# Optimization experiments

Hardware: AMD Instinct MI355X
Metric: run time of the kernel (lower is better)

## Reference

```python
import jax, jax.numpy as jnp
import numpy as np

H = 2048       # hidden_size
NH = 16        # num_attention_heads
HN = H // NH   # per-head dim = 128
B = 2
S = 2048
ALPHA = 32.0   # cogview pb-relax alpha


def setup_inputs() -> dict:
    key = jax.random.key(0)
    k1, k2, k3 = jax.random.split(key, 3)
    hidden_states = jax.random.normal(k1, (B, S, H), dtype=jnp.float32)
    # causal lower-triangular float mask [1,1,s,s]
    ltor_mask = jnp.tril(jnp.ones((S, S), dtype=jnp.float32))[None, None]
    # fused QKV projection params (torch Linear: y = x @ W.T + b)
    lim_qkv = 1.0 / np.sqrt(H)
    W_qkv = jax.random.uniform(k2, (3 * H, H), jnp.float32, -lim_qkv, lim_qkv)
    b_qkv = jnp.zeros((3 * H,), jnp.float32)
    W_out = jax.random.uniform(k3, (H, H), jnp.float32, -lim_qkv, lim_qkv)
    b_out = jnp.zeros((H,), jnp.float32)
    return {"hidden_states": hidden_states, "ltor_mask": ltor_mask,
            "W_qkv": W_qkv, "b_qkv": b_qkv, "W_out": W_out, "b_out": b_out}


def reference(hidden_states, ltor_mask, W_qkv, b_qkv, W_out, b_out):
    b, s, h = hidden_states.shape
    # fused QKV projection: [b,s,3h]
    qkv = hidden_states @ W_qkv.T + b_qkv
    q, k, v = jnp.split(qkv, 3, axis=-1)
    # [b,s,h] -> [b,n,s,hn]
    def heads(t):
        return t.reshape(b, s, NH, HN).transpose(0, 2, 1, 3)
    q, k, v = heads(q), heads(k), heads(v)
    # cogview_pb_relax: scale query before matmul
    scores = jnp.einsum('bnqd,bnkd->bnqk', q / jnp.sqrt(jnp.float32(HN)), k)
    mask = ltor_mask[:, :, -scores.shape[-2]:]
    scores = scores * mask - 10000.0 * (1.0 - mask)
    # pb-relax max rescaling (max is detached)
    scaled = scores / ALPHA
    maxes = jax.lax.stop_gradient(jnp.max(scaled.reshape(b, NH, -1), axis=-1))
    scores = (scaled - maxes[:, :, None, None]) * ALPHA
    probs = jax.nn.softmax(scores, axis=-1)
    ctx = jnp.einsum('bnqk,bnkd->bnqd', probs, v)
    ctx = ctx.transpose(0, 2, 1, 3).reshape(b, s, h)
    out = ctx @ W_out.T + b_out
    return out
```

## Files before the change

kernel.cpp:

```cpp
#include <hip/hip_runtime.h>

typedef __bf16 bf16;
typedef bf16 bf16x4 __attribute__((ext_vector_type(4)));
typedef bf16 bf16x8 __attribute__((ext_vector_type(8)));
typedef unsigned short u16x8 __attribute__((ext_vector_type(8)));
typedef float f32x4 __attribute__((ext_vector_type(4)));

#define Bb 2
#define Ss 2048
#define Hh 2048
#define NHh 16
#define HNd 128
#define H3 6144
#define Mm 4096
#define SCALE_QK 0.08838834764831843f

__device__ __forceinline__ void async_copy16(void* lds, const void* g) {
  __builtin_amdgcn_global_load_lds(
      (const __attribute__((address_space(1))) unsigned int*)g,
      (__attribute__((address_space(3))) unsigned int*)lds, 16, 0, 0);
}

template <int N>
__device__ __forceinline__ void waitvm() {
  if constexpr (N == 0) asm volatile("s_waitcnt vmcnt(0)" ::: "memory");
  else if constexpr (N == 2) asm volatile("s_waitcnt vmcnt(2)" ::: "memory");
  else if constexpr (N == 3) asm volatile("s_waitcnt vmcnt(3)" ::: "memory");
}

__device__ __forceinline__ void cvt4(const float* in, bf16* out, int i) {
  float4 v = *reinterpret_cast<const float4*>(in + i);
  bf16x4 o;
  o[0] = (bf16)v.x; o[1] = (bf16)v.y; o[2] = (bf16)v.z; o[3] = (bf16)v.w;
  *reinterpret_cast<bf16x4*>(out + i) = o;
}

__global__ __launch_bounds__(256) void cvt3_kernel(
    const float* __restrict__ s0, bf16* __restrict__ d0, int n0,
    const float* __restrict__ s1, bf16* __restrict__ d1, int n1,
    const float* __restrict__ s2, bf16* __restrict__ d2, int n2) {
  int i = (blockIdx.x * 256 + threadIdx.x) * 4;
  if (i < n0) cvt4(s0, d0, i);
  else if ((i -= n0) < n1) cvt4(s1, d1, i);
  else if ((i -= n1) < n2) cvt4(s2, d2, i);
}

template <int NJ>
struct GFrags {
  bf16x8 af[2][2];
  bf16x8 bfr[NJ][2];
};

template <int NJ, int MP, int RDB>
__device__ __forceinline__ void g_reads(const bf16* asb, const bf16* bsb,
                                        int lm, int lg, int wm, int wn,
                                        GFrags<NJ>& f) {
  if (RDB) {
#pragma unroll
    for (int nj = 0; nj < NJ; ++nj)
#pragma unroll
      for (int kk = 0; kk < 2; ++kk) {
        const int row = wn * (NJ * 16) + nj * 16 + lm;
        f.bfr[nj][kk] = *reinterpret_cast<const bf16x8*>(
            (const char*)bsb + row * 128 + ((kk * 64 + lg * 16) ^ ((lm & 7) << 4)));
      }
  }
#pragma unroll
  for (int i = 0; i < 2; ++i)
#pragma unroll
    for (int kk = 0; kk < 2; ++kk) {
      const int row = wm * 128 + (MP * 2 + i) * 16 + lm;
      f.af[i][kk] = *reinterpret_cast<const bf16x8*>(
          (const char*)asb + row * 128 + ((kk * 64 + lg * 16) ^ ((lm & 7) << 4)));
    }
}

template <int NJ, int MP>
__device__ __forceinline__ void g_mfma(const GFrags<NJ>& f, f32x4 (&acc)[8][NJ]) {
#pragma unroll
  for (int kk = 0; kk < 2; ++kk)
#pragma unroll
    for (int i = 0; i < 2; ++i)
#pragma unroll
      for (int nj = 0; nj < NJ; ++nj)
        acc[MP * 2 + i][nj] = __builtin_amdgcn_mfma_f32_16x16x32_bf16(
            f.af[i][kk], f.bfr[nj][kk], acc[MP * 2 + i][nj], 0, 0, 0);
}

template <int NJ, int OUT_F32>
__global__ __launch_bounds__(512, 2) void gemmW_kernel(
    const bf16* __restrict__ A, const bf16* __restrict__ Bw,
    const float* __restrict__ bias, void* __restrict__ Cout,
    int M, int N, int K) {
  __shared__ __align__(16) bf16 As[2][256 * 64];
  __shared__ __align__(16) bf16 Bs[2][NJ * 64 * 64];

  const int tid = threadIdx.x;
  const int lane = tid & 63;
  const int w = tid >> 6;
  const int wm = w >> 2, wn = w & 3;
  const int lm = lane & 15, lg = lane >> 4;
  const int srow = lane >> 3;
  const int sslot = lane & 7;

  const int id = blockIdx.y * gridDim.x + blockIdx.x;
  const int cpx = gridDim.x >> 3;
  const int xcd = id & 7, rem = id >> 3;
  const int bx = xcd * cpx + rem % cpx;
  const int by = rem / cpx;
  const int m0 = by * 256, n0 = bx * (NJ * 64);

  auto stageA = [&](int b, int t) {
#pragma unroll
    for (int l = 0; l < 4; ++l) {
      const int r = l * 64 + w * 8 + srow;
      async_copy16((char*)&As[b][0] + l * 8192 + w * 1024,
                   A + (size_t)(m0 + r) * K + t * 64 + (sslot ^ srow) * 8);
    }
  };
  auto stageB = [&](int b, int t) {
#pragma unroll
    for (int l = 0; l < NJ; ++l) {
      const int r = l * 64 + w * 8 + srow;
      async_copy16((char*)&Bs[b][0] + l * 8192 + w * 1024,
                   Bw + (size_t)(n0 + r) * K + t * 64 + (sslot ^ srow) * 8);
    }
  };

  f32x4 acc[8][NJ] = {};
  GFrags<NJ> f;

#define PHASE(BS, MP, RDB, VM, ...)                                            \
  do {                                                                         \
    g_reads<NJ, MP, RDB>(&As[BS][0], &Bs[BS][0], lm, lg, wm, wn, f);           \
    __VA_ARGS__;                                                               \
    __builtin_amdgcn_s_barrier();                                              \
    __builtin_amdgcn_s_setprio(1);                                             \
    g_mfma<NJ, MP>(f, acc);                                                    \
    __builtin_amdgcn_s_setprio(0);                                             \
    waitvm<(VM)>();                                                            \
    __builtin_amdgcn_s_barrier();                                              \
  } while (0)

  const int nt = K >> 6;
  stageB(0, 0);
  stageA(0, 0);
  stageB(1, 1);
  waitvm<NJ>();
  __builtin_amdgcn_s_barrier();

#pragma unroll 1
  for (int t = 0; t < nt - 2; t += 2) {
    PHASE(0, 0, 1, 9, stageA(1, t + 1));
    PHASE(0, 1, 0, 9, stageB(0, t + 2));
    PHASE(0, 2, 0, 9, );
    PHASE(0, 3, 0, NJ, );
    PHASE(1, 0, 1, 9, stageA(0, t + 2));
    PHASE(1, 1, 0, 9, stageB(1, t + 3));
    PHASE(1, 2, 0, 9, );
    PHASE(1, 3, 0, NJ, );
  }
  PHASE(0, 0, 1, 9, stageA(1, nt - 1));
  PHASE(0, 1, 0, 9, );
  PHASE(0, 2, 0, 9, );
  PHASE(0, 3, 0, 0, );
  PHASE(1, 0, 1, 9, );
  PHASE(1, 1, 0, 9, );
  PHASE(1, 2, 0, 9, );
  PHASE(1, 3, 0, 9, );
#undef PHASE

#pragma unroll
  for (int mi = 0; mi < 8; ++mi) {
#pragma unroll
    for (int nj = 0; nj < NJ; ++nj) {
      const int col = n0 + wn * (NJ * 16) + nj * 16 + lm;
      const float bv = bias[col];
      const int r0 = m0 + wm * 128 + mi * 16 + lg * 4;
#pragma unroll
      for (int r = 0; r < 4; ++r) {
        const float v = acc[mi][nj][r] + bv;
        if (OUT_F32)
          reinterpret_cast<float*>(Cout)[(size_t)(r0 + r) * N + col] = v;
        else
          reinterpret_cast<bf16*>(Cout)[(size_t)(r0 + r) * N + col] = (bf16)v;
      }
    }
  }
}

__device__ __forceinline__ void attn_tile(
    const char* ksb, const char* vtb, bf16* psw,
    const bf16x8* qf, f32x4* acc, float* mrow, float* lrow,
    int qr0, int kv0, bool diag, int lm, int lg) {
  float p[4][4];
#pragma unroll
  for (int kt = 0; kt < 4; ++kt) {
    f32x4 s = {};
    const int r = kt * 16 + lm;
#pragma unroll
    for (int kk = 0; kk < 4; ++kk) {
      bf16x8 kf = *reinterpret_cast<const bf16x8*>(
          ksb + r * 256 + ((kk * 64 + lg * 16) ^ ((lm & 7) << 4)));
      s = __builtin_amdgcn_mfma_f32_16x16x32_bf16(qf[kk], kf, s, 0, 0, 0);
    }
    if (diag) {
      const int col = kv0 + kt * 16 + lm;
#pragma unroll
      for (int rr = 0; rr < 4; ++rr)
        p[kt][rr] = (col <= qr0 + lg * 4 + rr) ? s[rr] * SCALE_QK : -3.0e38f;
    } else {
#pragma unroll
      for (int rr = 0; rr < 4; ++rr) p[kt][rr] = s[rr] * SCALE_QK;
    }
  }
#pragma unroll
  for (int rr = 0; rr < 4; ++rr) {
    float pm = fmaxf(fmaxf(p[0][rr], p[1][rr]), fmaxf(p[2][rr], p[3][rr]));
#pragma unroll
    for (int off = 1; off < 16; off <<= 1) pm = fmaxf(pm, __shfl_xor(pm, off));
    const float mnew = fmaxf(mrow[rr], pm);
    const float sc = __expf(mrow[rr] - mnew);
    mrow[rr] = mnew;
    float sum = 0.f;
#pragma unroll
    for (int kt = 0; kt < 4; ++kt) { p[kt][rr] = __expf(p[kt][rr] - mnew); sum += p[kt][rr]; }
#pragma unroll
    for (int off = 1; off < 16; off <<= 1) sum += __shfl_xor(sum, off);
    lrow[rr] = lrow[rr] * sc + sum;
#pragma unroll
    for (int dt = 0; dt < 8; ++dt) acc[dt][rr] *= sc;
  }
#pragma unroll
  for (int kt = 0; kt < 4; ++kt)
#pragma unroll
    for (int rr = 0; rr < 4; ++rr)
      psw[(lg * 4 + rr) * 72 + kt * 16 + lm] = (bf16)p[kt][rr];
  __syncthreads();
#pragma unroll
  for (int kb = 0; kb < 2; ++kb) {
    bf16x8 pa = *reinterpret_cast<const bf16x8*>(&psw[lm * 72 + kb * 32 + lg * 8]);
#pragma unroll
    for (int dt = 0; dt < 8; ++dt) {
      const int d = dt * 16 + lm;
      bf16x8 vf = *reinterpret_cast<const bf16x8*>(
          vtb + d * 128 + ((kb * 64 + lg * 16) ^ (((dt * 2 + (lm >> 3)) & 7) << 4)));
      acc[dt] = __builtin_amdgcn_mfma_f32_16x16x32_bf16(pa, vf, acc[dt], 0, 0, 0);
    }
  }
}

__global__ __launch_bounds__(256, 2) void attn_kernel(const bf16* __restrict__ qkv,
                                                      bf16* __restrict__ ctx) {
  __shared__ __align__(16) bf16 Ks[2][64 * 128];
  __shared__ __align__(16) bf16 Vt[2][128 * 64];
  __shared__ __align__(16) bf16 Ps[4 * 16 * 72];

  const int tid = threadIdx.x;
  const int lane = tid & 63;
  const int w = tid >> 6;
  const int lm = lane & 15;
  const int lg = lane >> 4;
  const int bid = blockIdx.x;
  const int xcd = bid & 7;
  const int rr_ = bid >> 3;
  const int bh = xcd * 4 + (rr_ & 3);
  const int pr = rr_ >> 2;
  const int b = bh >> 4;
  const int h = bh & 15;
  const int qtA = 31 - pr;
  const int qtB = pr;

  const size_t rs = H3;
  const bf16* qbase = qkv + (size_t)b * Ss * rs + (size_t)h * HNd;
  const bf16* kbase = qbase + Hh;
  const bf16* vbase = qbase + 2 * Hh;

  const int qrA = qtA * 64 + w * 16;
  const int qrB = qtB * 64 + w * 16;

  bf16x8 qfA[4], qfB[4];
#pragma unroll
  for (int kk = 0; kk < 4; ++kk) {
    qfA[kk] = *reinterpret_cast<const bf16x8*>(qbase + (size_t)(qrA + lm) * rs + kk * 32 + lg * 8);
    qfB[kk] = *reinterpret_cast<const bf16x8*>(qbase + (size_t)(qrB + lm) * rs + kk * 32 + lg * 8);
  }

  f32x4 accA[8] = {}, accB[8] = {};
  float mA[4], lA[4], mB[4], lB[4];
#pragma unroll
  for (int r = 0; r < 4; ++r) { mA[r] = mB[r] = -3.0e38f; lA[r] = lB[r] = 0.f; }

  bf16* psw = Ps + w * 16 * 72;

  auto stageK = [&](char* ksb, int kv0) {
#pragma unroll
    for (int c = 0; c < 4; ++c) {
      const int ci = c * 4 + w;
      const int row = ci * 4 + lg;
      async_copy16(ksb + ci * 1024,
                   kbase + (size_t)(kv0 + row) * rs + (lm ^ (row & 7)) * 8);
    }
  };
  auto loadV = [&](int kv0, bf16x8* vr) {
#pragma unroll
    for (int jj = 0; jj < 2; ++jj) {
      const int idx = jj * 256 + tid;
      const int pair = idx >> 4;
      const int d8 = idx & 15;
      vr[jj * 2 + 0] = *reinterpret_cast<const bf16x8*>(
          vbase + (size_t)(kv0 + pair * 2) * rs + d8 * 8);
      vr[jj * 2 + 1] = *reinterpret_cast<const bf16x8*>(
          vbase + (size_t)(kv0 + pair * 2 + 1) * rs + d8 * 8);
    }
  };
  auto writeV = [&](char* vtb, const bf16x8* vr) {
#pragma unroll
    for (int jj = 0; jj < 2; ++jj) {
      const int idx = jj * 256 + tid;
      const int pair = idx >> 4;
      const int d8 = idx & 15;
      const u16x8 lo = (u16x8)vr[jj * 2 + 0];
      const u16x8 hi = (u16x8)vr[jj * 2 + 1];
#pragma unroll
      for (int e = 0; e < 8; ++e) {
        const unsigned pk = (unsigned)lo[e] | ((unsigned)hi[e] << 16);
        *reinterpret_cast<unsigned*>(
            vtb + (d8 * 8 + e) * 128 + ((pair * 4) ^ ((d8 & 7) << 4))) = pk;
      }
    }
  };

  bf16x8 vr[4];
  stageK((char*)Ks[0], 0);
  loadV(0, vr);
  writeV((char*)Vt[0], vr);
  __syncthreads();

  const int nkv = qtA + 1;
  for (int t = 0; t < nkv; ++t) {
    const int cur = t & 1;
    const bool pf = (t + 1 < nkv);
    if (pf) {
      stageK((char*)Ks[cur ^ 1], (t + 1) * 64);
      loadV((t + 1) * 64, vr);
    }
    const int kv0 = t * 64;
    attn_tile((char*)Ks[cur], (char*)Vt[cur], psw, qfA, accA, mA, lA, qrA, kv0,
              t == qtA, lm, lg);
    if (t <= qtB)
      attn_tile((char*)Ks[cur], (char*)Vt[cur], psw, qfB, accB, mB, lB, qrB, kv0,
                t == qtB, lm, lg);
    if (pf) writeV((char*)Vt[cur ^ 1], vr);
    __syncthreads();
  }

  bf16* cbase = ctx + (size_t)b * Ss * Hh + (size_t)h * HNd;
#pragma unroll
  for (int dt = 0; dt < 8; ++dt)
#pragma unroll
    for (int r = 0; r < 4; ++r) {
      cbase[(size_t)(qrA + lg * 4 + r) * Hh + dt * 16 + lm] = (bf16)(accA[dt][r] / lA[r]);
      cbase[(size_t)(qrB + lg * 4 + r) * Hh + dt * 16 + lm] = (bf16)(accB[dt][r] / lB[r]);
    }
}

extern "C" void kernel_launch(void* const* d_in, const int* in_sizes, int n_in,
                              void* d_out, int out_size, void* d_ws, size_t ws_size,
                              hipStream_t stream) {
  const float* hidden = (const float*)d_in[0];
  const float* Wqkv = (const float*)d_in[2];
  const float* bqkv = (const float*)d_in[3];
  const float* Wout = (const float*)d_in[4];
  const float* bout = (const float*)d_in[5];
  float* out = (float*)d_out;

  char* ws = (char*)d_ws;
  bf16* hid_bf = (bf16*)ws;  ws += (size_t)Mm * Hh * 2;
  bf16* wqkv_bf = (bf16*)ws; ws += (size_t)H3 * Hh * 2;
  bf16* wout_bf = (bf16*)ws; ws += (size_t)Hh * Hh * 2;
  bf16* qkv_bf = (bf16*)ws;  ws += (size_t)Mm * H3 * 2;
  bf16* ctx_bf = (bf16*)ws;  ws += (size_t)Mm * Hh * 2;

  const int n0 = Mm * Hh, n1 = H3 * Hh, n2 = Hh * Hh;
  cvt3_kernel<<<((n0 + n1 + n2) / 4 + 255) / 256, 256, 0, stream>>>(
      hidden, hid_bf, n0, Wqkv, wqkv_bf, n1, Wout, wout_bf, n2);

  gemmW_kernel<3, 0><<<dim3(H3 / 192, Mm / 256), 512, 0, stream>>>(
      hid_bf, wqkv_bf, bqkv, qkv_bf, Mm, H3, Hh);
  attn_kernel<<<dim3(512), 256, 0, stream>>>(qkv_bf, ctx_bf);
  gemmW_kernel<2, 1><<<dim3(Hh / 128, Mm / 256), 512, 0, stream>>>(
      ctx_bf, wout_bf, bout, out, Mm, Hh, Hh);
}
```

Baseline: 269.8 us.

## Pad transposed V tile in LDS and replace P-tile barrier with fence

The transposed V tile in shared memory changes from an XOR-swizzled 128-byte row layout to a padded 136-byte row stride. Each thread now loads four consecutive kv rows and writes 8-byte packed pairs instead of 4-byte ones. The PV MFMA reads now use two 8-byte loads per fragment instead of one 16-byte load. The block-wide barrier after writing the per-wave P tile becomes a block-scope fence, since each wave only reads its own P slice. The fence relies on intra-wave ordering, and the split loads may add LDS instructions.

```diff
diff --git a/kernel.cpp b/kernel.cpp
--- a/kernel.cpp
+++ b/kernel.cpp
@@ -236,15 +236,17 @@
 #pragma unroll
     for (int rr = 0; rr < 4; ++rr)
       psw[(lg * 4 + rr) * 72 + kt * 16 + lm] = (bf16)p[kt][rr];
-  __syncthreads();
+  __threadfence_block();
 #pragma unroll
   for (int kb = 0; kb < 2; ++kb) {
     bf16x8 pa = *reinterpret_cast<const bf16x8*>(&psw[lm * 72 + kb * 32 + lg * 8]);
 #pragma unroll
     for (int dt = 0; dt < 8; ++dt) {
       const int d = dt * 16 + lm;
-      bf16x8 vf = *reinterpret_cast<const bf16x8*>(
-          vtb + d * 128 + ((kb * 64 + lg * 16) ^ (((dt * 2 + (lm >> 3)) & 7) << 4)));
+      const char* vp = vtb + d * 136 + kb * 64 + lg * 16;
+      bf16x4 vlo = *reinterpret_cast<const bf16x4*>(vp);
+      bf16x4 vhi = *reinterpret_cast<const bf16x4*>(vp + 8);
+      bf16x8 vf = __builtin_shufflevector(vlo, vhi, 0, 1, 2, 3, 4, 5, 6, 7);
       acc[dt] = __builtin_amdgcn_mfma_f32_16x16x32_bf16(pa, vf, acc[dt], 0, 0, 0);
     }
   }
@@ -253,7 +255,7 @@
 __global__ __launch_bounds__(256, 2) void attn_kernel(const bf16* __restrict__ qkv,
                                                       bf16* __restrict__ ctx) {
   __shared__ __align__(16) bf16 Ks[2][64 * 128];
-  __shared__ __align__(16) bf16 Vt[2][128 * 64];
+  __shared__ __align__(16) bf16 Vt[2][128 * 68];
   __shared__ __align__(16) bf16 Ps[4 * 16 * 72];
 
   const int tid = threadIdx.x;
@@ -303,31 +305,24 @@
     }
   };
   auto loadV = [&](int kv0, bf16x8* vr) {
-#pragma unroll
-    for (int jj = 0; jj < 2; ++jj) {
-      const int idx = jj * 256 + tid;
-      const int pair = idx >> 4;
-      const int d8 = idx & 15;
-      vr[jj * 2 + 0] = *reinterpret_cast<const bf16x8*>(
-          vbase + (size_t)(kv0 + pair * 2) * rs + d8 * 8);
-      vr[jj * 2 + 1] = *reinterpret_cast<const bf16x8*>(
-          vbase + (size_t)(kv0 + pair * 2 + 1) * rs + d8 * 8);
-    }
+    const int kvq = tid >> 4;
+    const int d8 = tid & 15;
+#pragma unroll
+    for (int j = 0; j < 4; ++j)
+      vr[j] = *reinterpret_cast<const bf16x8*>(
+          vbase + (size_t)(kv0 + kvq * 4 + j) * rs + d8 * 8);
   };
   auto writeV = [&](char* vtb, const bf16x8* vr) {
-#pragma unroll
-    for (int jj = 0; jj < 2; ++jj) {
-      const int idx = jj * 256 + tid;
-      const int pair = idx >> 4;
-      const int d8 = idx & 15;
-      const u16x8 lo = (u16x8)vr[jj * 2 + 0];
-      const u16x8 hi = (u16x8)vr[jj * 2 + 1];
-#pragma unroll
-      for (int e = 0; e < 8; ++e) {
-        const unsigned pk = (unsigned)lo[e] | ((unsigned)hi[e] << 16);
-        *reinterpret_cast<unsigned*>(
-            vtb + (d8 * 8 + e) * 128 + ((pair * 4) ^ ((d8 & 7) << 4))) = pk;
-      }
+    const int kvq = tid >> 4;
+    const int d8 = tid & 15;
+    const u16x8 a = (u16x8)vr[0], bq = (u16x8)vr[1];
+    const u16x8 c = (u16x8)vr[2], dq = (u16x8)vr[3];
+#pragma unroll
+    for (int e = 0; e < 8; ++e) {
+      uint2 pk;
+      pk.x = (unsigned)a[e] | ((unsigned)bq[e] << 16);
+      pk.y = (unsigned)c[e] | ((unsigned)dq[e] << 16);
+      *reinterpret_cast<uint2*>(vtb + (d8 * 8 + e) * 136 + kvq * 8) = pk;
     }
   };
 
```

New measurement: 273.7 us. No clear change (+1.5%).

## Use exp2 softmax with lazy rescaling and MFMA-computed row sums in attention

Applied to the files above, without the earlier changes.

Folds log2(e) into the QK scale so exponentials use exp2. The running-max update and accumulator rescale are skipped unless a row's tile max exceeds the stored max by a threshold, checked wave-uniformly. The softmax denominator is accumulated with an MFMA against a ones vector instead of shuffle reductions. This removes per-tile shuffles and rescale multiplies, at the cost of one extra MFMA and probabilities that may exceed 1 by a bounded factor.

```diff
diff --git a/kernel.cpp b/kernel.cpp
--- a/kernel.cpp
+++ b/kernel.cpp
@@ -13,7 +13,8 @@
 #define HNd 128
 #define H3 6144
 #define Mm 4096
-#define SCALE_QK 0.08838834764831843f
+#define SCALE_LOG2 0.12752039136902522f
+#define DTHR 8.0f
 
 __device__ __forceinline__ void async_copy16(void* lds, const void* g) {
   __builtin_amdgcn_global_load_lds(
@@ -191,7 +192,7 @@
 
 __device__ __forceinline__ void attn_tile(
     const char* ksb, const char* vtb, bf16* psw,
-    const bf16x8* qf, f32x4* acc, float* mrow, float* lrow,
+    const bf16x8* qf, f32x4* acc, f32x4& accl, float* mrow,
     int qr0, int kv0, bool diag, int lm, int lg) {
   float p[4][4];
 #pragma unroll
@@ -208,38 +209,50 @@
       const int col = kv0 + kt * 16 + lm;
 #pragma unroll
       for (int rr = 0; rr < 4; ++rr)
-        p[kt][rr] = (col <= qr0 + lg * 4 + rr) ? s[rr] * SCALE_QK : -3.0e38f;
+        p[kt][rr] = (col <= qr0 + lg * 4 + rr) ? s[rr] * SCALE_LOG2 : -3.0e38f;
     } else {
 #pragma unroll
-      for (int rr = 0; rr < 4; ++rr) p[kt][rr] = s[rr] * SCALE_QK;
-    }
-  }
+      for (int rr = 0; rr < 4; ++rr) p[kt][rr] = s[rr] * SCALE_LOG2;
+    }
+  }
+  float pm4[4];
 #pragma unroll
   for (int rr = 0; rr < 4; ++rr) {
     float pm = fmaxf(fmaxf(p[0][rr], p[1][rr]), fmaxf(p[2][rr], p[3][rr]));
 #pragma unroll
     for (int off = 1; off < 16; off <<= 1) pm = fmaxf(pm, __shfl_xor(pm, off));
-    const float mnew = fmaxf(mrow[rr], pm);
-    const float sc = __expf(mrow[rr] - mnew);
-    mrow[rr] = mnew;
-    float sum = 0.f;
-#pragma unroll
-    for (int kt = 0; kt < 4; ++kt) { p[kt][rr] = __expf(p[kt][rr] - mnew); sum += p[kt][rr]; }
-#pragma unroll
-    for (int off = 1; off < 16; off <<= 1) sum += __shfl_xor(sum, off);
-    lrow[rr] = lrow[rr] * sc + sum;
-#pragma unroll
-    for (int dt = 0; dt < 8; ++dt) acc[dt][rr] *= sc;
-  }
+    pm4[rr] = pm;
+  }
+  const bool need = (pm4[0] > mrow[0] + DTHR) || (pm4[1] > mrow[1] + DTHR) ||
+                    (pm4[2] > mrow[2] + DTHR) || (pm4[3] > mrow[3] + DTHR);
+  if (__any(need)) {
+#pragma unroll
+    for (int rr = 0; rr < 4; ++rr) {
+      const float mnew = fmaxf(mrow[rr], pm4[rr]);
+      const float sc = exp2f(mrow[rr] - mnew);
+      mrow[rr] = mnew;
+      accl[rr] *= sc;
+#pragma unroll
+      for (int dt = 0; dt < 8; ++dt) acc[dt][rr] *= sc;
+    }
+  }
+#pragma unroll
+  for (int kt = 0; kt < 4; ++kt)
+#pragma unroll
+    for (int rr = 0; rr < 4; ++rr)
+      p[kt][rr] = exp2f(p[kt][rr] - mrow[rr]);
 #pragma unroll
   for (int kt = 0; kt < 4; ++kt)
 #pragma unroll
     for (int rr = 0; rr < 4; ++rr)
       psw[(lg * 4 + rr) * 72 + kt * 16 + lm] = (bf16)p[kt][rr];
   __syncthreads();
+  const bf16 one = (bf16)1.0f;
+  const bf16x8 ones = {one, one, one, one, one, one, one, one};
 #pragma unroll
   for (int kb = 0; kb < 2; ++kb) {
     bf16x8 pa = *reinterpret_cast<const bf16x8*>(&psw[lm * 72 + kb * 32 + lg * 8]);
+    accl = __builtin_amdgcn_mfma_f32_16x16x32_bf16(pa, ones, accl, 0, 0, 0);
 #pragma unroll
     for (int dt = 0; dt < 8; ++dt) {
       const int d = dt * 16 + lm;
@@ -287,9 +300,10 @@
   }
 
   f32x4 accA[8] = {}, accB[8] = {};
-  float mA[4], lA[4], mB[4], lB[4];
-#pragma unroll
-  for (int r = 0; r < 4; ++r) { mA[r] = mB[r] = -3.0e38f; lA[r] = lB[r] = 0.f; }
+  f32x4 aclA = {}, aclB = {};
+  float mA[4], mB[4];
+#pragma unroll
+  for (int r = 0; r < 4; ++r) { mA[r] = mB[r] = -3.0e38f; }
 
   bf16* psw = Ps + w * 16 * 72;
 
@@ -346,10 +360,10 @@
       loadV((t + 1) * 64, vr);
     }
     const int kv0 = t * 64;
-    attn_tile((char*)Ks[cur], (char*)Vt[cur], psw, qfA, accA, mA, lA, qrA, kv0,
+    attn_tile((char*)Ks[cur], (char*)Vt[cur], psw, qfA, accA, aclA, mA, qrA, kv0,
               t == qtA, lm, lg);
     if (t <= qtB)
-      attn_tile((char*)Ks[cur], (char*)Vt[cur], psw, qfB, accB, mB, lB, qrB, kv0,
+      attn_tile((char*)Ks[cur], (char*)Vt[cur], psw, qfB, accB, aclB, mB, qrB, kv0,
                 t == qtB, lm, lg);
     if (pf) writeV((char*)Vt[cur ^ 1], vr);
     __syncthreads();
@@ -360,8 +374,8 @@
   for (int dt = 0; dt < 8; ++dt)
 #pragma unroll
     for (int r = 0; r < 4; ++r) {
-      cbase[(size_t)(qrA + lg * 4 + r) * Hh + dt * 16 + lm] = (bf16)(accA[dt][r] / lA[r]);
-      cbase[(size_t)(qrB + lg * 4 + r) * Hh + dt * 16 + lm] = (bf16)(accB[dt][r] / lB[r]);
+      cbase[(size_t)(qrA + lg * 4 + r) * Hh + dt * 16 + lm] = (bf16)(accA[dt][r] / aclA[r]);
+      cbase[(size_t)(qrB + lg * 4 + r) * Hh + dt * 16 + lm] = (bf16)(accB[dt][r] / aclB[r]);
     }
 }
 
```

New measurement: 261.2 us. 1.03x faster.
